# Optimization experiments

Hardware: AMD Instinct MI355X
Metric: run time of the kernel (lower is better)

The kernel has to match this reference:

```python
import jax, jax.numpy as jnp
import numpy as np

N = 100000
E = 1600000
DIM = 64
HEADS = 8
HEAD_DIM = DIM // HEADS
LN_EPS = 1e-5
NORM_EPS = 1e-12


def setup_inputs() -> dict:
    key = jax.random.key(0)
    ks = jax.random.split(key, 5)
    x = jax.random.normal(ks[0], (N, DIM), dtype=jnp.float32)
    edge_index = jax.random.randint(ks[1], (2, E), 0, N, dtype=jnp.int32)
    W_w = jax.random.normal(ks[2], (DIM, DIM), dtype=jnp.float32) * (1.0 / np.sqrt(DIM))
    W_b = jax.random.normal(ks[3], (DIM,), dtype=jnp.float32) * 0.01
    a = jax.random.normal(ks[4], (HEADS, 2 * HEAD_DIM), dtype=jnp.float32) * 0.1
    ln_scale = jnp.ones((DIM,), dtype=jnp.float32)
    ln_bias = jnp.zeros((DIM,), dtype=jnp.float32)
    return {"x": x, "edge_index": edge_index, "W_w": W_w, "W_b": W_b,
            "a": a, "ln_scale": ln_scale, "ln_bias": ln_bias}


def reference(x, edge_index, W_w, W_b, a, ln_scale, ln_bias):
    n = x.shape[0]
    # Linear (dropout = identity in eval), reshape to heads
    h = (x @ W_w.T + W_b).reshape(n, HEADS, HEAD_DIM)          # [N,H,D]
    src, dst = edge_index[0], edge_index[1]
    hs = h[src]                                                 # [E,H,D]
    hd = h[dst]                                                 # [E,H,D]
    a_src, a_dst = a[:, :HEAD_DIM], a[:, HEAD_DIM:]             # [H,D] each
    # (a * cat(hs, hd)).sum(-1) split over the two halves
    alpha = jnp.einsum('ehd,hd->eh', hs, a_src) + jnp.einsum('ehd,hd->eh', hd, a_dst)
    alpha = jnp.where(alpha >= 0, alpha, 0.2 * alpha)           # LeakyReLU(0.2)
    alpha = jax.nn.softmax(alpha, axis=1)                       # NOTE: over heads, as in source
    msg = alpha[..., None] * hd                                 # [E,H,D]
    out = jax.ops.segment_sum(msg, src, num_segments=n)         # scatter-add to src nodes
    out = out.reshape(n, DIM)
    # residual + LayerNorm
    y = out + x
    mu = jnp.mean(y, axis=-1, keepdims=True)
    var = jnp.mean((y - mu) ** 2, axis=-1, keepdims=True)
    y = (y - mu) * jax.lax.rsqrt(var + LN_EPS) * ln_scale + ln_bias
    # F.normalize(p=2, dim=-1)
    norm = jnp.sqrt(jnp.sum(y * y, axis=-1, keepdims=True))
    return y / jnp.maximum(norm, NORM_EPS)
```

## Files before the change

### kernel.cpp

```cpp
#include <hip/hip_runtime.h>
#include <hip/hip_fp16.h>
#include <math.h>

#define N_NODES 100000
#define N_EDGES 1600000
#define LN_EPS 1e-5f
#define NORM_EPS 1e-12f
#define ROWS_PER_BLOCK 32
#define GEMM_BLOCKS (N_NODES / ROWS_PER_BLOCK)
#define WSTRIDE 66
#define WB 64
#define NBKT ((N_NODES + WB - 1) / WB)
#define BIN_TILE 8192
#define BIN_BLOCKS ((N_EDGES + BIN_TILE - 1) / BIN_TILE)
#define GB_LDS 25088

__global__ __launch_bounds__(256) void k_gemm_bin(
    const float* __restrict__ x, const float* __restrict__ W,
    const float* __restrict__ b, const float* __restrict__ a,
    __half* __restrict__ h16,
    float* __restrict__ s_src, float* __restrict__ s_dst,
    const int* __restrict__ ei, int* __restrict__ gbin,
    unsigned int* __restrict__ staged)
{
    extern __shared__ char smem[];
    const int tid = threadIdx.x;

    if (blockIdx.x < BIN_BLOCKS) {
        int* hist = (int*)smem;
        int* base = hist + NBKT;
        for (int bb = tid; bb < NBKT; bb += 256) hist[bb] = 0;
        __syncthreads();

        const int e0 = blockIdx.x * BIN_TILE;
        #pragma unroll 4
        for (int j = 0; j < 32; ++j) {
            const int e = e0 + j * 256 + tid;
            if (e < N_EDGES) atomicAdd(&hist[ei[e] >> 6], 1);
        }
        __syncthreads();
        for (int bb = tid; bb < NBKT; bb += 256)
            if (hist[bb]) base[bb] = atomicAdd(&gbin[bb], hist[bb]);
        __syncthreads();
        #pragma unroll 4
        for (int j = 0; j < 32; ++j) {
            const int e = e0 + j * 256 + tid;
            if (e < N_EDGES) {
                const int s = ei[e];
                const int d = ei[N_EDGES + e];
                const int idx = atomicAdd(&base[s >> 6], 1);
                staged[(size_t)idx] = (unsigned int)((s & 63) | (d << 6));
            }
        }
        return;
    }

    float* WL = (float*)smem;
    float* xs = WL + 64 * WSTRIDE;
    const int lane = tid & 63;
    const int wv   = tid >> 6;

    for (int idx = tid * 4; idx < 64 * 64; idx += 256 * 4) {
        const float4 w = *(const float4*)(W + idx);
        const int c = idx >> 6, k = idx & 63;
        WL[c * WSTRIDE + k + 0] = w.x;
        WL[c * WSTRIDE + k + 1] = w.y;
        WL[c * WSTRIDE + k + 2] = w.z;
        WL[c * WSTRIDE + k + 3] = w.w;
    }
    const int row0 = (blockIdx.x - BIN_BLOCKS) * ROWS_PER_BLOCK;
    for (int idx = tid * 4; idx < ROWS_PER_BLOCK * 64; idx += 256 * 4)
        *(float4*)(xs + idx) = *(const float4*)(x + (size_t)row0 * 64 + idx);
    __syncthreads();

    const float bias = b[lane];
    float acc[8];
    #pragma unroll
    for (int r = 0; r < 8; ++r) acc[r] = bias;

    const int rbase = wv * 8;
    const float* wrow = WL + lane * WSTRIDE;
    const float* xrow = xs + rbase * 64;
    #pragma unroll 1
    for (int kk = 0; kk < 64; kk += 4) {
        const float2 w01 = *(const float2*)(wrow + kk);
        const float2 w23 = *(const float2*)(wrow + kk + 2);
        #pragma unroll
        for (int r = 0; r < 8; ++r) {
            const float4 xq = *(const float4*)(xrow + r * 64 + kk);
            acc[r] += xq.x * w01.x + xq.y * w01.y + xq.z * w23.x + xq.w * w23.y;
        }
    }

    const float asrc = a[(lane >> 3) * 16 + (lane & 7)];
    const float adst = a[(lane >> 3) * 16 + 8 + (lane & 7)];
    #pragma unroll
    for (int r = 0; r < 8; ++r) {
        const int row = row0 + rbase + r;
        const float v = acc[r];
        h16[(size_t)row * 64 + lane] = __float2half_rn(v);
        float p = v * asrc, q = v * adst;
        p += __shfl_xor(p, 1);  q += __shfl_xor(q, 1);
        p += __shfl_xor(p, 2);  q += __shfl_xor(q, 2);
        p += __shfl_xor(p, 4);  q += __shfl_xor(q, 4);
        if ((lane & 7) == 0) {
            s_src[row * 8 + (lane >> 3)] = p;
            s_dst[row * 8 + (lane >> 3)] = q;
        }
    }
}

__global__ __launch_bounds__(1024) void k_hist(
    const int* __restrict__ ei, int* __restrict__ bhist)
{
    __shared__ int hist[NBKT];
    const int tid = threadIdx.x;
    for (int b = tid; b < NBKT; b += 1024) hist[b] = 0;
    __syncthreads();
    const int e0 = blockIdx.x * BIN_TILE;
    #pragma unroll
    for (int j = 0; j < 8; ++j) {
        const int e = e0 + j * 1024 + tid;
        if (e < N_EDGES) atomicAdd(&hist[ei[e] >> 6], 1);
    }
    __syncthreads();
    for (int b = tid; b < NBKT; b += 1024)
        if (hist[b]) atomicAdd(&bhist[b], hist[b]);
}

__global__ __launch_bounds__(1024) void k_bscan(
    const int* __restrict__ bhist, int* __restrict__ bucket_base,
    int* __restrict__ gbin)
{
    __shared__ int wsum[16];
    const int tid = threadIdx.x, lane = tid & 63, wv = tid >> 6;

    int v = (tid < NBKT) ? bhist[tid] : 0;
    int sc = v;
    #pragma unroll
    for (int off = 1; off < 64; off <<= 1) {
        int t = __shfl_up(sc, off);
        if (lane >= off) sc += t;
    }
    if (lane == 63) wsum[wv] = sc;
    __syncthreads();
    if (tid < 16) {
        int ws = wsum[tid];
        #pragma unroll
        for (int off = 1; off < 16; off <<= 1) {
            int t = __shfl_up(ws, off);
            if (tid >= off) ws += t;
        }
        wsum[tid] = ws;
    }
    __syncthreads();
    const int pref0 = wv ? wsum[wv - 1] : 0;
    const int ex0 = pref0 + sc - v;
    if (tid < NBKT) { bucket_base[tid] = ex0; gbin[tid] = ex0; }
    const int T1 = wsum[15];
    __syncthreads();

    const int i2 = 1024 + tid;
    int v2 = (i2 < NBKT) ? bhist[i2] : 0;
    int sc2 = v2;
    #pragma unroll
    for (int off = 1; off < 64; off <<= 1) {
        int t = __shfl_up(sc2, off);
        if (lane >= off) sc2 += t;
    }
    if (lane == 63) wsum[wv] = sc2;
    __syncthreads();
    if (tid < 16) {
        int ws = wsum[tid];
        #pragma unroll
        for (int off = 1; off < 16; off <<= 1) {
            int t = __shfl_up(ws, off);
            if (tid >= off) ws += t;
        }
        wsum[tid] = ws;
    }
    __syncthreads();
    const int pref1 = wv ? wsum[wv - 1] : 0;
    const int ex1 = T1 + pref1 + sc2 - v2;
    if (i2 < NBKT) { bucket_base[i2] = ex1; gbin[i2] = ex1; }
    if (tid == 0) bucket_base[NBKT] = N_EDGES;
}

__global__ __launch_bounds__(1024) void k_place(
    const int* __restrict__ bucket_base, const unsigned int* __restrict__ staged,
    const float* __restrict__ s_src, const float* __restrict__ s_dst,
    int* __restrict__ row_ptr, int* __restrict__ dst_sorted,
    __half* __restrict__ alpha16)
{
    __shared__ int cnt[WB];
    __shared__ int cur[WB];
    const int g   = blockIdx.x;
    const int n0  = g * WB;
    const int tid = threadIdx.x;
    if (tid < WB) cnt[tid] = 0;
    __syncthreads();
    const int beg = bucket_base[g];
    const int end = bucket_base[g + 1];

    for (int j = beg + tid; j < end; j += 1024)
        atomicAdd(&cnt[staged[j] & 63u], 1);
    __syncthreads();
    if (tid < WB) {
        const int c = cnt[tid];
        int sc = c;
        #pragma unroll
        for (int off = 1; off < 64; off <<= 1) {
            int t = __shfl_up(sc, off);
            if (tid >= off) sc += t;
        }
        const int rp = beg + sc - c;
        cur[tid] = rp;
        if (n0 + tid < N_NODES) row_ptr[n0 + tid] = rp;
    }
    if (g == NBKT - 1 && tid == 0) row_ptr[N_NODES] = N_EDGES;
    __syncthreads();

    for (int j = beg + tid; j < end; j += 1024) {
        const unsigned int w = staged[j];
        const int srcl = (int)(w & 63u);
        const int dst  = (int)(w >> 6);

        const float4 a0 = *(const float4*)(s_src + (size_t)(n0 + srcl) * 8);
        const float4 a1 = *(const float4*)(s_src + (size_t)(n0 + srcl) * 8 + 4);
        const float4 b0 = *(const float4*)(s_dst + (size_t)dst * 8);
        const float4 b1 = *(const float4*)(s_dst + (size_t)dst * 8 + 4);
        float sc[8] = {a0.x + b0.x, a0.y + b0.y, a0.z + b0.z, a0.w + b0.w,
                       a1.x + b1.x, a1.y + b1.y, a1.z + b1.z, a1.w + b1.w};
        float m = -1e30f;
        #pragma unroll
        for (int h = 0; h < 8; ++h) {
            sc[h] = (sc[h] >= 0.f) ? sc[h] : 0.2f * sc[h];
            m = fmaxf(m, sc[h]);
        }
        float sum = 0.f;
        #pragma unroll
        for (int h = 0; h < 8; ++h) { sc[h] = __expf(sc[h] - m); sum += sc[h]; }
        const float inv = 1.f / sum;
        unsigned int q[4];
        #pragma unroll
        for (int jj = 0; jj < 4; ++jj) {
            const unsigned short lo = __half_as_ushort(__float2half_rn(sc[2*jj]   * inv));
            const unsigned short hi = __half_as_ushort(__float2half_rn(sc[2*jj+1] * inv));
            q[jj] = (unsigned int)lo | ((unsigned int)hi << 16);
        }

        const int slot = atomicAdd(&cur[srcl], 1);
        dst_sorted[slot] = dst;
        *(uint4*)(alpha16 + (size_t)slot * 8) = make_uint4(q[0], q[1], q[2], q[3]);
    }
}

__global__ __launch_bounds__(256) void k_gather(
    const int* __restrict__ row_ptr, const int* __restrict__ dst_sorted,
    const __half* __restrict__ alpha16, const __half* __restrict__ h16,
    const float* __restrict__ x, const float* __restrict__ ln_scale,
    const float* __restrict__ ln_bias, float* __restrict__ out)
{
    const int i = __builtin_amdgcn_readfirstlane(
        blockIdx.x * 4 + (threadIdx.x >> 6));
    if (i >= N_NODES) return;
    const int lane = threadIdx.x & 63;
    const int head = lane >> 3;

    const int beg = row_ptr[i];
    const int end = row_ptr[i + 1];
    const float xres = x[(size_t)i * 64 + lane];

    float acc = 0.f;
    int e = beg;
    for (; e + 7 < end; e += 8) {
        int d[8];
        #pragma unroll
        for (int j = 0; j < 8; ++j) d[j] = dst_sorted[e + j];
        float al[8];
        #pragma unroll
        for (int j = 0; j < 8; ++j)
            al[j] = __half2float(alpha16[(size_t)(e + j) * 8 + head]);
        float hv[8];
        #pragma unroll
        for (int j = 0; j < 8; ++j)
            hv[j] = __half2float(h16[(size_t)d[j] * 64 + lane]);
        #pragma unroll
        for (int j = 0; j < 8; ++j) acc = fmaf(al[j], hv[j], acc);
    }
    for (; e + 3 < end; e += 4) {
        int d[4];
        #pragma unroll
        for (int j = 0; j < 4; ++j) d[j] = dst_sorted[e + j];
        float al[4];
        #pragma unroll
        for (int j = 0; j < 4; ++j)
            al[j] = __half2float(alpha16[(size_t)(e + j) * 8 + head]);
        float hv[4];
        #pragma unroll
        for (int j = 0; j < 4; ++j)
            hv[j] = __half2float(h16[(size_t)d[j] * 64 + lane]);
        #pragma unroll
        for (int j = 0; j < 4; ++j) acc = fmaf(al[j], hv[j], acc);
    }
    for (; e < end; ++e)
        acc = fmaf(__half2float(alpha16[(size_t)e * 8 + head]),
                   __half2float(h16[(size_t)dst_sorted[e] * 64 + lane]), acc);

    float v = acc + xres;
    float s = v;
    #pragma unroll
    for (int off = 1; off < 64; off <<= 1) s += __shfl_xor(s, off);
    const float mu = s * (1.f / 64.f);
    const float d = v - mu;
    float vs = d * d;
    #pragma unroll
    for (int off = 1; off < 64; off <<= 1) vs += __shfl_xor(vs, off);
    const float var = vs * (1.f / 64.f);
    float y = d * rsqrtf(var + LN_EPS) * ln_scale[lane] + ln_bias[lane];
    float ss = y * y;
    #pragma unroll
    for (int off = 1; off < 64; off <<= 1) ss += __shfl_xor(ss, off);
    const float norm = sqrtf(ss);
    out[(size_t)i * 64 + lane] = y / fmaxf(norm, NORM_EPS);
}

extern "C" void kernel_launch(void* const* d_in, const int* in_sizes, int n_in,
                              void* d_out, int out_size, void* d_ws, size_t ws_size,
                              hipStream_t stream)
{
    const float* x        = (const float*)d_in[0];
    const int*   ei       = (const int*)d_in[1];
    const float* W        = (const float*)d_in[2];
    const float* b        = (const float*)d_in[3];
    const float* a        = (const float*)d_in[4];
    const float* ln_scale = (const float*)d_in[5];
    const float* ln_bias  = (const float*)d_in[6];
    float* out = (float*)d_out;

    char* ws = (char*)d_ws;
    size_t off = 0;
    auto alloc = [&](size_t bytes) {
        void* p = ws + off;
        off = (off + bytes + 255) & ~(size_t)255;
        return p;
    };
    __half* h16        = (__half*)alloc((size_t)N_NODES * 64 * 2);
    float*  s_src      = (float*) alloc((size_t)N_NODES * 8 * 4);
    float*  s_dst      = (float*) alloc((size_t)N_NODES * 8 * 4);
    int*    bhist      = (int*)   alloc((size_t)NBKT * 4);
    int*    bucket_base= (int*)   alloc((size_t)(NBKT + 1) * 4);
    int*    gbin       = (int*)   alloc((size_t)NBKT * 4);
    int*    row_ptr    = (int*)   alloc((size_t)(N_NODES + 1) * 4);
    unsigned int* staged = (unsigned int*)alloc((size_t)N_EDGES * 4);
    int*    dst_sorted = (int*)   alloc((size_t)N_EDGES * 4);
    __half* alpha16    = (__half*)alloc((size_t)N_EDGES * 8 * 2);

    hipMemsetAsync(bhist, 0, (size_t)NBKT * 4, stream);

    k_hist    <<<BIN_BLOCKS, 1024, 0, stream>>>(ei, bhist);
    k_bscan   <<<1, 1024, 0, stream>>>(bhist, bucket_base, gbin);
    k_gemm_bin<<<BIN_BLOCKS + GEMM_BLOCKS, 256, GB_LDS, stream>>>(
        x, W, b, a, h16, s_src, s_dst, ei, gbin, staged);
    k_place   <<<NBKT, 1024, 0, stream>>>(bucket_base, staged, s_src, s_dst,
                                          row_ptr, dst_sorted, alpha16);
    k_gather  <<<(N_NODES + 3) / 4, 256, 0, stream>>>(row_ptr, dst_sorted, alpha16,
                                                      h16, x, ln_scale, ln_bias, out);
}
```

Baseline: 214.6 us.

## Fuse edge placement and gather into one kernel using LDS-staged CSR buckets

Merges the per-bucket placement kernel with the gather/LayerNorm kernel. Each 64-node bucket now keeps its sorted destination indices and fp16 attention weights in LDS (up to a fixed capacity, spilling to global overflow buffers), and its 16 waves then each process 4 nodes directly from LDS. This removes the global write and re-read of dst_sorted and alpha16, plus one kernel launch. The cost is large LDS use per 1024-thread block, about 26 KB, which limits occupancy, and less parallelism in the gather phase since each wave now handles 4 nodes serially. There is also a slow scalar overflow path for buckets larger than the capacity.

```diff
diff --git a/kernel.cpp b/kernel.cpp
--- a/kernel.cpp
+++ b/kernel.cpp
@@ -14,6 +14,7 @@
 #define BIN_TILE 8192
 #define BIN_BLOCKS ((N_EDGES + BIN_TILE - 1) / BIN_TILE)
 #define GB_LDS 25088
+#define CAP 1280
 
 __global__ __launch_bounds__(256) void k_gemm_bin(
     const float* __restrict__ x, const float* __restrict__ W,
@@ -186,38 +187,42 @@
     if (tid == 0) bucket_base[NBKT] = N_EDGES;
 }
 
-__global__ __launch_bounds__(1024) void k_place(
+__global__ __launch_bounds__(1024) void k_place_gather(
     const int* __restrict__ bucket_base, const unsigned int* __restrict__ staged,
     const float* __restrict__ s_src, const float* __restrict__ s_dst,
-    int* __restrict__ row_ptr, int* __restrict__ dst_sorted,
-    __half* __restrict__ alpha16)
-{
-    __shared__ int cnt[WB];
+    const __half* __restrict__ h16, const float* __restrict__ x,
+    const float* __restrict__ ln_scale, const float* __restrict__ ln_bias,
+    int* __restrict__ dst_ovf, __half* __restrict__ alpha_ovf,
+    float* __restrict__ out)
+{
+    __shared__ int lrow[WB + 1];
     __shared__ int cur[WB];
+    __shared__ unsigned int dstl[CAP];
+    __shared__ uint4 alds[CAP];
+
     const int g   = blockIdx.x;
     const int n0  = g * WB;
     const int tid = threadIdx.x;
-    if (tid < WB) cnt[tid] = 0;
+    if (tid < WB) cur[tid] = 0;
     __syncthreads();
     const int beg = bucket_base[g];
     const int end = bucket_base[g + 1];
 
     for (int j = beg + tid; j < end; j += 1024)
-        atomicAdd(&cnt[staged[j] & 63u], 1);
+        atomicAdd(&cur[staged[j] & 63u], 1);
     __syncthreads();
     if (tid < WB) {
-        const int c = cnt[tid];
+        const int c = cur[tid];
         int sc = c;
         #pragma unroll
         for (int off = 1; off < 64; off <<= 1) {
             int t = __shfl_up(sc, off);
             if (tid >= off) sc += t;
         }
-        const int rp = beg + sc - c;
-        cur[tid] = rp;
-        if (n0 + tid < N_NODES) row_ptr[n0 + tid] = rp;
-    }
-    if (g == NBKT - 1 && tid == 0) row_ptr[N_NODES] = N_EDGES;
+        lrow[tid] = sc - c;
+        cur[tid]  = sc - c;
+        if (tid == WB - 1) lrow[WB] = sc;
+    }
     __syncthreads();
 
     for (int j = beg + tid; j < end; j += 1024) {
@@ -249,80 +254,102 @@
             q[jj] = (unsigned int)lo | ((unsigned int)hi << 16);
         }
 
-        const int slot = atomicAdd(&cur[srcl], 1);
-        dst_sorted[slot] = dst;
-        *(uint4*)(alpha16 + (size_t)slot * 8) = make_uint4(q[0], q[1], q[2], q[3]);
-    }
-}
-
-__global__ __launch_bounds__(256) void k_gather(
-    const int* __restrict__ row_ptr, const int* __restrict__ dst_sorted,
-    const __half* __restrict__ alpha16, const __half* __restrict__ h16,
-    const float* __restrict__ x, const float* __restrict__ ln_scale,
-    const float* __restrict__ ln_bias, float* __restrict__ out)
-{
-    const int i = __builtin_amdgcn_readfirstlane(
-        blockIdx.x * 4 + (threadIdx.x >> 6));
-    if (i >= N_NODES) return;
-    const int lane = threadIdx.x & 63;
+        const int ls = atomicAdd(&cur[srcl], 1);
+        if (ls < CAP) {
+            dstl[ls] = (unsigned int)dst;
+            alds[ls] = make_uint4(q[0], q[1], q[2], q[3]);
+        } else {
+            dst_ovf[beg + ls] = dst;
+            *(uint4*)(alpha_ovf + (size_t)(beg + ls) * 8) =
+                make_uint4(q[0], q[1], q[2], q[3]);
+        }
+    }
+    __syncthreads();
+
+    const int lane = tid & 63;
+    const int wv   = tid >> 6;
     const int head = lane >> 3;
 
-    const int beg = row_ptr[i];
-    const int end = row_ptr[i + 1];
-    const float xres = x[(size_t)i * 64 + lane];
-
-    float acc = 0.f;
-    int e = beg;
-    for (; e + 7 < end; e += 8) {
-        int d[8];
-        #pragma unroll
-        for (int j = 0; j < 8; ++j) d[j] = dst_sorted[e + j];
-        float al[8];
-        #pragma unroll
-        for (int j = 0; j < 8; ++j)
-            al[j] = __half2float(alpha16[(size_t)(e + j) * 8 + head]);
-        float hv[8];
-        #pragma unroll
-        for (int j = 0; j < 8; ++j)
-            hv[j] = __half2float(h16[(size_t)d[j] * 64 + lane]);
-        #pragma unroll
-        for (int j = 0; j < 8; ++j) acc = fmaf(al[j], hv[j], acc);
-    }
-    for (; e + 3 < end; e += 4) {
-        int d[4];
-        #pragma unroll
-        for (int j = 0; j < 4; ++j) d[j] = dst_sorted[e + j];
-        float al[4];
-        #pragma unroll
-        for (int j = 0; j < 4; ++j)
-            al[j] = __half2float(alpha16[(size_t)(e + j) * 8 + head]);
-        float hv[4];
-        #pragma unroll
-        for (int j = 0; j < 4; ++j)
-            hv[j] = __half2float(h16[(size_t)d[j] * 64 + lane]);
-        #pragma unroll
-        for (int j = 0; j < 4; ++j) acc = fmaf(al[j], hv[j], acc);
-    }
-    for (; e < end; ++e)
-        acc = fmaf(__half2float(alpha16[(size_t)e * 8 + head]),
-                   __half2float(h16[(size_t)dst_sorted[e] * 64 + lane]), acc);
-
-    float v = acc + xres;
-    float s = v;
-    #pragma unroll
-    for (int off = 1; off < 64; off <<= 1) s += __shfl_xor(s, off);
-    const float mu = s * (1.f / 64.f);
-    const float d = v - mu;
-    float vs = d * d;
-    #pragma unroll
-    for (int off = 1; off < 64; off <<= 1) vs += __shfl_xor(vs, off);
-    const float var = vs * (1.f / 64.f);
-    float y = d * rsqrtf(var + LN_EPS) * ln_scale[lane] + ln_bias[lane];
-    float ss = y * y;
-    #pragma unroll
-    for (int off = 1; off < 64; off <<= 1) ss += __shfl_xor(ss, off);
-    const float norm = sqrtf(ss);
-    out[(size_t)i * 64 + lane] = y / fmaxf(norm, NORM_EPS);
+    #pragma unroll 1
+    for (int r = 0; r < 4; ++r) {
+        const int nl = wv * 4 + r;
+        const int i  = n0 + nl;
+        if (i >= N_NODES) continue;
+        const int bl = lrow[nl];
+        const int el = lrow[nl + 1];
+        const float xres = x[(size_t)i * 64 + lane];
+
+        float acc = 0.f;
+        if (el <= CAP) {
+            int e = bl;
+            for (; e + 7 < el; e += 8) {
+                int d[8];
+                #pragma unroll
+                for (int j = 0; j < 8; ++j)
+                    d[j] = __builtin_amdgcn_readfirstlane((int)dstl[e + j]);
+                float al[8];
+                #pragma unroll
+                for (int j = 0; j < 8; ++j)
+                    al[j] = __half2float(((const __half*)&alds[e + j])[head]);
+                float hv[8];
+                #pragma unroll
+                for (int j = 0; j < 8; ++j)
+                    hv[j] = __half2float(h16[(size_t)d[j] * 64 + lane]);
+                #pragma unroll
+                for (int j = 0; j < 8; ++j) acc = fmaf(al[j], hv[j], acc);
+            }
+            for (; e + 3 < el; e += 4) {
+                int d[4];
+                #pragma unroll
+                for (int j = 0; j < 4; ++j)
+                    d[j] = __builtin_amdgcn_readfirstlane((int)dstl[e + j]);
+                float al[4];
+                #pragma unroll
+                for (int j = 0; j < 4; ++j)
+                    al[j] = __half2float(((const __half*)&alds[e + j])[head]);
+                float hv[4];
+                #pragma unroll
+                for (int j = 0; j < 4; ++j)
+                    hv[j] = __half2float(h16[(size_t)d[j] * 64 + lane]);
+                #pragma unroll
+                for (int j = 0; j < 4; ++j) acc = fmaf(al[j], hv[j], acc);
+            }
+            for (; e < el; ++e) {
+                const int d = __builtin_amdgcn_readfirstlane((int)dstl[e]);
+                acc = fmaf(__half2float(((const __half*)&alds[e])[head]),
+                           __half2float(h16[(size_t)d * 64 + lane]), acc);
+            }
+        } else {
+            for (int e = bl; e < el; ++e) {
+                int d; float al;
+                if (e < CAP) {
+                    d  = (int)dstl[e];
+                    al = __half2float(((const __half*)&alds[e])[head]);
+                } else {
+                    d  = dst_ovf[beg + e];
+                    al = __half2float(alpha_ovf[(size_t)(beg + e) * 8 + head]);
+                }
+                acc = fmaf(al, __half2float(h16[(size_t)d * 64 + lane]), acc);
+            }
+        }
+
+        float v = acc + xres;
+        float s = v;
+        #pragma unroll
+        for (int off = 1; off < 64; off <<= 1) s += __shfl_xor(s, off);
+        const float mu = s * (1.f / 64.f);
+        const float dd = v - mu;
+        float vs = dd * dd;
+        #pragma unroll
+        for (int off = 1; off < 64; off <<= 1) vs += __shfl_xor(vs, off);
+        const float var = vs * (1.f / 64.f);
+        float y = dd * rsqrtf(var + LN_EPS) * ln_scale[lane] + ln_bias[lane];
+        float ss = y * y;
+        #pragma unroll
+        for (int off = 1; off < 64; off <<= 1) ss += __shfl_xor(ss, off);
+        const float norm = sqrtf(ss);
+        out[(size_t)i * 64 + lane] = y / fmaxf(norm, NORM_EPS);
+    }
 }
 
 extern "C" void kernel_launch(void* const* d_in, const int* in_sizes, int n_in,
@@ -351,19 +378,17 @@
     int*    bhist      = (int*)   alloc((size_t)NBKT * 4);
     int*    bucket_base= (int*)   alloc((size_t)(NBKT + 1) * 4);
     int*    gbin       = (int*)   alloc((size_t)NBKT * 4);
-    int*    row_ptr    = (int*)   alloc((size_t)(N_NODES + 1) * 4);
     unsigned int* staged = (unsigned int*)alloc((size_t)N_EDGES * 4);
-    int*    dst_sorted = (int*)   alloc((size_t)N_EDGES * 4);
-    __half* alpha16    = (__half*)alloc((size_t)N_EDGES * 8 * 2);
+    int*    dst_ovf    = (int*)   alloc((size_t)N_EDGES * 4);
+    __half* alpha_ovf  = (__half*)alloc((size_t)N_EDGES * 8 * 2);
 
     hipMemsetAsync(bhist, 0, (size_t)NBKT * 4, stream);
 
-    k_hist    <<<BIN_BLOCKS, 1024, 0, stream>>>(ei, bhist);
-    k_bscan   <<<1, 1024, 0, stream>>>(bhist, bucket_base, gbin);
-    k_gemm_bin<<<BIN_BLOCKS + GEMM_BLOCKS, 256, GB_LDS, stream>>>(
+    k_hist        <<<BIN_BLOCKS, 1024, 0, stream>>>(ei, bhist);
+    k_bscan       <<<1, 1024, 0, stream>>>(bhist, bucket_base, gbin);
+    k_gemm_bin    <<<BIN_BLOCKS + GEMM_BLOCKS, 256, GB_LDS, stream>>>(
         x, W, b, a, h16, s_src, s_dst, ei, gbin, staged);
-    k_place   <<<NBKT, 1024, 0, stream>>>(bucket_base, staged, s_src, s_dst,
-                                          row_ptr, dst_sorted, alpha16);
-    k_gather  <<<(N_NODES + 3) / 4, 256, 0, stream>>>(row_ptr, dst_sorted, alpha16,
-                                                      h16, x, ln_scale, ln_bias, out);
-}
+    k_place_gather<<<NBKT, 1024, 0, stream>>>(bucket_base, staged, s_src, s_dst,
+                                              h16, x, ln_scale, ln_bias,
+                                              dst_ovf, alpha_ovf, out);
+}
```

New measurement: 204.8 us (median of 3 runs). 4.6% less time.
